# Optimization experiments

Hardware: AMD Instinct MI355X
Metric: run time of the kernel (lower is better)

Reference implementation:

```python
import jax, jax.numpy as jnp
import numpy as np

N, D, V = 2048, 64, 2048


def setup_inputs() -> dict:
    key = jax.random.key(0)
    k_ids, k_emb, k_tree, k_map = jax.random.split(key, 4)
    language_ids = jax.random.randint(k_ids, (N,), 0, V)
    language_embeddings = jax.random.normal(k_emb, (N, D), dtype=jnp.float32)
    # symmetric distance tables, mimicking the symmetric try/except dict lookup
    t = jax.random.uniform(k_tree, (V, V), dtype=jnp.float32)
    tree_dist = (t + t.T) * 0.5
    m = jax.random.uniform(k_map, (V, V), dtype=jnp.float32)
    map_dist = (m + m.T) * 0.5
    return {
        "language_ids": language_ids,
        "language_embeddings": language_embeddings,
        "tree_dist": tree_dist,
        "map_dist": map_dist,
    }


def reference(language_ids, language_embeddings, tree_dist, map_dist):
    # pairwise mean-L1 distance between embeddings: [N, N]
    emb_dist = jnp.mean(
        jnp.abs(language_embeddings[:, None, :] - language_embeddings[None, :, :]),
        axis=-1,
    )
    # largest_value_map_dist as computed in __init__
    largest = jnp.max(map_dist)
    ii = language_ids[:, None]  # [N, 1]
    jj = language_ids[None, :]  # [1, N]
    metric = (tree_dist[ii, jj] + map_dist[ii, jj] / largest) * 0.5  # [N, N]
    # pairs with equal language ids are skipped in the original loop
    mask = (ii != jj).astype(emb_dist.dtype)
    per_pair = jnp.abs(emb_dist - metric) * mask
    return jnp.sum(per_pair) / jnp.sum(mask)
```

## Files before the change

### kernel.cpp

```cpp
#include <hip/hip_runtime.h>
#include <hip/hip_bf16.h>

#define NL 2048
#define DE 64
#define VV 2048
#define BI 64
#define BJ 32
#define NTI (NL / BI)
#define NTJ (NL / BJ)
#define NBLK 1056
#define STI 68
#define STJ 36


__global__ __launch_bounds__(1024) void prep_kernel(const int* __restrict__ ids,
                                                    const float4* __restrict__ m4,
                                                    float* __restrict__ pmax,
                                                    int* __restrict__ perm,
                                                    int* __restrict__ sids) {
    const int t = threadIdx.x;
    const int lane = t & 63, wave = t >> 6;
    const int b = blockIdx.x;

    if (b < 256) {
        const float4* p = m4 + (size_t)b * 4096;
        const float4 x0 = p[t], x1 = p[t + 1024], x2 = p[t + 2048], x3 = p[t + 3072];
        float v = fmaxf(fmaxf(fmaxf(x0.x, x0.y), fmaxf(x0.z, x0.w)),
                        fmaxf(fmaxf(x1.x, x1.y), fmaxf(x1.z, x1.w)));
        v = fmaxf(v, fmaxf(fmaxf(x2.x, x2.y), fmaxf(x2.z, x2.w)));
        v = fmaxf(v, fmaxf(fmaxf(x3.x, x3.y), fmaxf(x3.z, x3.w)));
        #pragma unroll
        for (int o = 32; o > 0; o >>= 1)
            v = fmaxf(v, __shfl_down(v, o));
        __shared__ float wl[16];
        if (lane == 0) wl[wave] = v;
        __syncthreads();
        if (t == 0) {
            float m = wl[0];
            #pragma unroll
            for (int i = 1; i < 16; ++i) m = fmaxf(m, wl[i]);
            pmax[b] = m;
        }
    } else {
        __shared__ unsigned hist[VV];
        __shared__ unsigned offs[VV];
        __shared__ unsigned wtot[16];
        __shared__ unsigned wexc[16];
        hist[2 * t] = 0u; hist[2 * t + 1] = 0u;
        __syncthreads();
        const int id0 = ids[2 * t], id1 = ids[2 * t + 1];
        atomicAdd(&hist[id0], 1u);
        atomicAdd(&hist[id1], 1u);
        __syncthreads();
        const unsigned h0 = hist[2 * t], h1 = hist[2 * t + 1];
        const unsigned s = h0 + h1;
        unsigned ps = s;
        #pragma unroll
        for (int o = 1; o < 64; o <<= 1) {
            unsigned u = __shfl_up(ps, o);
            if (lane >= o) ps += u;
        }
        if (lane == 63) wtot[wave] = ps;
        __syncthreads();
        if (wave == 0 && lane < 16) {
            unsigned v = wtot[lane];
            unsigned pv = v;
            #pragma unroll
            for (int o = 1; o < 16; o <<= 1) {
                unsigned u = __shfl_up(pv, o);
                if (lane >= o) pv += u;
            }
            wexc[lane] = pv - v;
        }
        __syncthreads();
        const unsigned ex = wexc[wave] + ps - s;
        offs[2 * t]     = ex;
        offs[2 * t + 1] = ex + h0;
        __syncthreads();
        unsigned p0 = atomicAdd(&offs[id0], 1u);
        perm[p0] = 2 * t;     sids[p0] = id0;
        unsigned p1 = atomicAdd(&offs[id1], 1u);
        perm[p1] = 2 * t + 1; sids[p1] = id1;
    }
}

__global__ __launch_bounds__(256) void loss_kernel(
    const float* __restrict__ emb,
    const float* __restrict__ tree, const float* __restrict__ mapd,
    const int* __restrict__ perm, const int* __restrict__ sids,
    const float* __restrict__ pmax,
    float* __restrict__ psum, unsigned* __restrict__ pcnt)
{
    const int t = threadIdx.x;

    const int L = blockIdx.x;
    int bi = (int)((65.0f - sqrtf(4225.0f - 4.0f * (float)L)) * 0.5f);
    if (bi > NTI - 1) bi = NTI - 1;
    if (bi < 0) bi = 0;
    while (65 * bi - bi * bi > L) --bi;
    while (65 * (bi + 1) - (bi + 1) * (bi + 1) <= L) ++bi;
    const int bj = 2 * bi + (L - (65 * bi - bi * bi));

    __shared__ __align__(16) float Eit[DE][STI];
    __shared__ __align__(16) float Ejt[DE][STJ];
    __shared__ int idi[BI];
    __shared__ int idj[BJ];
    __shared__ float wm[4];

    float pv = pmax[t];

    {
        const int r  = t & 63;
        const int c0 = (t >> 6) << 4;
        const int gi = perm[bi * BI + r];
        const float4* pa = (const float4*)(emb + (size_t)gi * DE + c0);
        float4 a0 = pa[0], a1 = pa[1], a2 = pa[2], a3 = pa[3];
        Eit[c0 + 0][r]  = a0.x; Eit[c0 + 1][r]  = a0.y; Eit[c0 + 2][r]  = a0.z; Eit[c0 + 3][r]  = a0.w;
        Eit[c0 + 4][r]  = a1.x; Eit[c0 + 5][r]  = a1.y; Eit[c0 + 6][r]  = a1.z; Eit[c0 + 7][r]  = a1.w;
        Eit[c0 + 8][r]  = a2.x; Eit[c0 + 9][r]  = a2.y; Eit[c0 + 10][r] = a2.z; Eit[c0 + 11][r] = a2.w;
        Eit[c0 + 12][r] = a3.x; Eit[c0 + 13][r] = a3.y; Eit[c0 + 14][r] = a3.z; Eit[c0 + 15][r] = a3.w;

        const int rj  = t & 31;
        const int cj0 = (t >> 5) << 3;
        const int gj = perm[bj * BJ + rj];
        const float4* pb = (const float4*)(emb + (size_t)gj * DE + cj0);
        float4 b0 = pb[0], b1 = pb[1];
        Ejt[cj0 + 0][rj] = b0.x; Ejt[cj0 + 1][rj] = b0.y; Ejt[cj0 + 2][rj] = b0.z; Ejt[cj0 + 3][rj] = b0.w;
        Ejt[cj0 + 4][rj] = b1.x; Ejt[cj0 + 5][rj] = b1.y; Ejt[cj0 + 6][rj] = b1.z; Ejt[cj0 + 7][rj] = b1.w;

        if (t < BI)            idi[t] = sids[bi * BI + t];
        else if (t < BI + BJ)  idj[t - BI] = sids[bj * BJ + (t - BI)];
    }
    #pragma unroll
    for (int o = 32; o > 0; o >>= 1)
        pv = fmaxf(pv, __shfl_down(pv, o));
    if ((t & 63) == 0) wm[t >> 6] = pv;
    __syncthreads();

    const float inv = 1.0f / fmaxf(fmaxf(wm[0], wm[1]), fmaxf(wm[2], wm[3]));

    const int i0 = (t >> 4) * 4;
    const int j0 = (t & 15) * 2;

    int ia[4], ja[2];
    #pragma unroll
    for (int s = 0; s < 4; ++s) ia[s] = idi[i0 + s];
    #pragma unroll
    for (int c = 0; c < 2; ++c) ja[c] = idj[j0 + c];
    float tg[4][2], mg[4][2];
    #pragma unroll
    for (int s = 0; s < 4; ++s)
        #pragma unroll
        for (int c = 0; c < 2; ++c) {
            const int off = ia[s] * VV + ja[c];
            tg[s][c] = tree[off];
            mg[s][c] = mapd[off];
        }

    float acc[4][2];
    #pragma unroll
    for (int s = 0; s < 4; ++s) { acc[s][0] = 0.0f; acc[s][1] = 0.0f; }

    #pragma unroll 2
    for (int k = 0; k < 16; ++k) {
        #pragma unroll
        for (int q = 0; q < 4; ++q) {
            const int d = 4 * k + q;
            const float4 a = *(const float4*)&Eit[d][i0];
            const float2 b = *(const float2*)&Ejt[d][j0];
            acc[0][0] += fabsf(a.x - b.x); acc[0][1] += fabsf(a.x - b.y);
            acc[1][0] += fabsf(a.y - b.x); acc[1][1] += fabsf(a.y - b.y);
            acc[2][0] += fabsf(a.z - b.x); acc[2][1] += fabsf(a.z - b.y);
            acc[3][0] += fabsf(a.w - b.x); acc[3][1] += fabsf(a.w - b.y);
        }
    }

    float pp = 0.0f;
    unsigned cnt = 0;
    #pragma unroll
    for (int s = 0; s < 4; ++s) {
        const int posi = bi * BI + i0 + s;
        #pragma unroll
        for (int c = 0; c < 2; ++c) {
            const int posj = bj * BJ + j0 + c;
            if (posi < posj && ia[s] != ja[c]) {
                const float metric = (tg[s][c] + mg[s][c] * inv) * 0.5f;
                pp += 2.0f * fabsf(acc[s][c] * (1.0f / (float)DE) - metric);
                cnt += 2u;
            }
        }
    }

    #pragma unroll
    for (int o = 32; o > 0; o >>= 1) {
        pp  += __shfl_down(pp, o);
        cnt += __shfl_down(cnt, o);
    }
    __shared__ float    wsum_l[4];
    __shared__ unsigned wcnt_l[4];
    if ((t & 63) == 0) { wsum_l[t >> 6] = pp; wcnt_l[t >> 6] = cnt; }
    __syncthreads();
    if (t == 0) {
        psum[L] = wsum_l[0] + wsum_l[1] + wsum_l[2] + wsum_l[3];
        pcnt[L] = wcnt_l[0] + wcnt_l[1] + wcnt_l[2] + wcnt_l[3];
    }
}

__global__ __launch_bounds__(1024) void finalize_kernel(const float* __restrict__ psum,
                                                        const unsigned* __restrict__ pcnt,
                                                        float* __restrict__ out) {
    const int t = threadIdx.x;
    const int lane = t & 63, wave = t >> 6;
    double s = 0.0;
    unsigned c = 0;
    for (int i = t; i < NBLK; i += 1024) { s += (double)psum[i]; c += pcnt[i]; }
    #pragma unroll
    for (int o = 32; o > 0; o >>= 1) {
        s += __shfl_down(s, o);
        c += __shfl_down(c, o);
    }
    __shared__ double   sl[16];
    __shared__ unsigned cl[16];
    if (lane == 0) { sl[wave] = s; cl[wave] = c; }
    __syncthreads();
    if (t == 0) {
        double   S = sl[0];
        unsigned C = cl[0];
        #pragma unroll
        for (int i = 1; i < 16; ++i) { S += sl[i]; C += cl[i]; }
        out[0] = (float)(S / (double)C);
    }
}

extern "C" void kernel_launch(void* const* d_in, const int* in_sizes, int n_in,
                              void* d_out, int out_size, void* d_ws, size_t ws_size,
                              hipStream_t stream) {
    const int*   ids  = (const int*)d_in[0];
    const float* emb  = (const float*)d_in[1];
    const float* tree = (const float*)d_in[2];
    const float* mapd = (const float*)d_in[3];
    float* out = (float*)d_out;

    float*    pmax = (float*)d_ws;
    int*      perm = (int*)((char*)d_ws + 1024);
    int*      sids = (int*)((char*)d_ws + 9216);
    float*    psum = (float*)((char*)d_ws + 17408);
    unsigned* pcnt = (unsigned*)((char*)d_ws + 21632);

    prep_kernel<<<257, 1024, 0, stream>>>(ids, (const float4*)mapd, pmax, perm, sids);

    loss_kernel<<<NBLK, 256, 0, stream>>>(emb, tree, mapd, perm, sids, pmax, psum, pcnt);

    finalize_kernel<<<1, 1024, 0, stream>>>(psum, pcnt, out);
}
```

Measured before the change: 98.79 us.

## Enlarge i-tile to 128 with 4x4 register blocking and hoisted gathers

Doubles the i tile (BI 64→128) so each thread computes a 4x4 block of pairs instead of 4x2, halving the number of triangular blocks and increasing LDS reuse per load. The id and distance-table gathers are now issued straight from global memory before the embedding staging, rather than after the barrier, so their latency overlaps the shared-memory fill. Mask and metric are precomputed into a bitmask with popcount for the count. In exchange register pressure rises (a 3-waves hint is added), and fewer blocks means less parallelism across CUs.

```diff
diff --git a/kernel.cpp b/kernel.cpp
--- a/kernel.cpp
+++ b/kernel.cpp
@@ -4,12 +4,11 @@
 #define NL 2048
 #define DE 64
 #define VV 2048
-#define BI 64
+#define BI 128
 #define BJ 32
-#define NTI (NL / BI)
-#define NTJ (NL / BJ)
-#define NBLK 1056
-#define STI 68
+#define NTI 16
+#define NBLK 544
+#define STI 132
 #define STJ 36
 
 
@@ -84,7 +83,7 @@
     }
 }
 
-__global__ __launch_bounds__(256) void loss_kernel(
+__global__ __launch_bounds__(256, 3) void loss_kernel(
     const float* __restrict__ emb,
     const float* __restrict__ tree, const float* __restrict__ mapd,
     const int* __restrict__ perm, const int* __restrict__ sids,
@@ -94,24 +93,42 @@
     const int t = threadIdx.x;
 
     const int L = blockIdx.x;
-    int bi = (int)((65.0f - sqrtf(4225.0f - 4.0f * (float)L)) * 0.5f);
+    int bi = (int)((66.0f - sqrtf(4356.0f - 8.0f * (float)L)) * 0.25f);
     if (bi > NTI - 1) bi = NTI - 1;
     if (bi < 0) bi = 0;
-    while (65 * bi - bi * bi > L) --bi;
-    while (65 * (bi + 1) - (bi + 1) * (bi + 1) <= L) ++bi;
-    const int bj = 2 * bi + (L - (65 * bi - bi * bi));
+    while (66 * bi - 2 * bi * bi > L) --bi;
+    while (66 * (bi + 1) - 2 * (bi + 1) * (bi + 1) <= L) ++bi;
+    const int bj = 4 * bi + (L - (66 * bi - 2 * bi * bi));
+
+    const int i0 = (t >> 3) * 4;
+    const int j0 = (t & 7) * 4;
+
+    int ia[4], ja[4];
+    #pragma unroll
+    for (int s = 0; s < 4; ++s) ia[s] = sids[bi * BI + i0 + s];
+    #pragma unroll
+    for (int c = 0; c < 4; ++c) ja[c] = sids[bj * BJ + j0 + c];
+    float tg[4][4], mg[4][4];
+    #pragma unroll
+    for (int s = 0; s < 4; ++s)
+        #pragma unroll
+        for (int c = 0; c < 4; ++c) {
+            const int off = ia[s] * VV + ja[c];
+            tg[s][c] = tree[off];
+            mg[s][c] = mapd[off];
+        }
 
     __shared__ __align__(16) float Eit[DE][STI];
     __shared__ __align__(16) float Ejt[DE][STJ];
-    __shared__ int idi[BI];
-    __shared__ int idj[BJ];
     __shared__ float wm[4];
 
     float pv = pmax[t];
 
-    {
-        const int r  = t & 63;
-        const int c0 = (t >> 6) << 4;
+    #pragma unroll
+    for (int s = 0; s < 2; ++s) {
+        const int idx = t + 256 * s;
+        const int r  = idx & 127;
+        const int c0 = (idx >> 7) * 16;
         const int gi = perm[bi * BI + r];
         const float4* pa = (const float4*)(emb + (size_t)gi * DE + c0);
         float4 a0 = pa[0], a1 = pa[1], a2 = pa[2], a3 = pa[3];
@@ -119,17 +136,17 @@
         Eit[c0 + 4][r]  = a1.x; Eit[c0 + 5][r]  = a1.y; Eit[c0 + 6][r]  = a1.z; Eit[c0 + 7][r]  = a1.w;
         Eit[c0 + 8][r]  = a2.x; Eit[c0 + 9][r]  = a2.y; Eit[c0 + 10][r] = a2.z; Eit[c0 + 11][r] = a2.w;
         Eit[c0 + 12][r] = a3.x; Eit[c0 + 13][r] = a3.y; Eit[c0 + 14][r] = a3.z; Eit[c0 + 15][r] = a3.w;
-
-        const int rj  = t & 31;
-        const int cj0 = (t >> 5) << 3;
-        const int gj = perm[bj * BJ + rj];
-        const float4* pb = (const float4*)(emb + (size_t)gj * DE + cj0);
-        float4 b0 = pb[0], b1 = pb[1];
-        Ejt[cj0 + 0][rj] = b0.x; Ejt[cj0 + 1][rj] = b0.y; Ejt[cj0 + 2][rj] = b0.z; Ejt[cj0 + 3][rj] = b0.w;
-        Ejt[cj0 + 4][rj] = b1.x; Ejt[cj0 + 5][rj] = b1.y; Ejt[cj0 + 6][rj] = b1.z; Ejt[cj0 + 7][rj] = b1.w;
-
-        if (t < BI)            idi[t] = sids[bi * BI + t];
-        else if (t < BI + BJ)  idj[t - BI] = sids[bj * BJ + (t - BI)];
+    }
+    if (t < 128) {
+        const int r  = t & 31;
+        const int c0 = (t >> 5) * 16;
+        const int gj = perm[bj * BJ + r];
+        const float4* pb = (const float4*)(emb + (size_t)gj * DE + c0);
+        float4 b0 = pb[0], b1 = pb[1], b2 = pb[2], b3 = pb[3];
+        Ejt[c0 + 0][r]  = b0.x; Ejt[c0 + 1][r]  = b0.y; Ejt[c0 + 2][r]  = b0.z; Ejt[c0 + 3][r]  = b0.w;
+        Ejt[c0 + 4][r]  = b1.x; Ejt[c0 + 5][r]  = b1.y; Ejt[c0 + 6][r]  = b1.z; Ejt[c0 + 7][r]  = b1.w;
+        Ejt[c0 + 8][r]  = b2.x; Ejt[c0 + 9][r]  = b2.y; Ejt[c0 + 10][r] = b2.z; Ejt[c0 + 11][r] = b2.w;
+        Ejt[c0 + 12][r] = b3.x; Ejt[c0 + 13][r] = b3.y; Ejt[c0 + 14][r] = b3.z; Ejt[c0 + 15][r] = b3.w;
     }
     #pragma unroll
     for (int o = 32; o > 0; o >>= 1)
@@ -139,27 +156,24 @@
 
     const float inv = 1.0f / fmaxf(fmaxf(wm[0], wm[1]), fmaxf(wm[2], wm[3]));
 
-    const int i0 = (t >> 4) * 4;
-    const int j0 = (t & 15) * 2;
-
-    int ia[4], ja[2];
-    #pragma unroll
-    for (int s = 0; s < 4; ++s) ia[s] = idi[i0 + s];
-    #pragma unroll
-    for (int c = 0; c < 2; ++c) ja[c] = idj[j0 + c];
-    float tg[4][2], mg[4][2];
+    float met[4][4];
+    unsigned mbits = 0u;
+    #pragma unroll
+    for (int s = 0; s < 4; ++s) {
+        const int posi = bi * BI + i0 + s;
+        #pragma unroll
+        for (int c = 0; c < 4; ++c) {
+            met[s][c] = 0.5f * (tg[s][c] + mg[s][c] * inv);
+            const int posj = bj * BJ + j0 + c;
+            if (posi < posj && ia[s] != ja[c]) mbits |= 1u << (s * 4 + c);
+        }
+    }
+
+    float acc[4][4];
     #pragma unroll
     for (int s = 0; s < 4; ++s)
         #pragma unroll
-        for (int c = 0; c < 2; ++c) {
-            const int off = ia[s] * VV + ja[c];
-            tg[s][c] = tree[off];
-            mg[s][c] = mapd[off];
-        }
-
-    float acc[4][2];
-    #pragma unroll
-    for (int s = 0; s < 4; ++s) { acc[s][0] = 0.0f; acc[s][1] = 0.0f; }
+        for (int c = 0; c < 4; ++c) acc[s][c] = 0.0f;
 
     #pragma unroll 2
     for (int k = 0; k < 16; ++k) {
@@ -167,29 +181,26 @@
         for (int q = 0; q < 4; ++q) {
             const int d = 4 * k + q;
             const float4 a = *(const float4*)&Eit[d][i0];
-            const float2 b = *(const float2*)&Ejt[d][j0];
+            const float4 b = *(const float4*)&Ejt[d][j0];
             acc[0][0] += fabsf(a.x - b.x); acc[0][1] += fabsf(a.x - b.y);
+            acc[0][2] += fabsf(a.x - b.z); acc[0][3] += fabsf(a.x - b.w);
             acc[1][0] += fabsf(a.y - b.x); acc[1][1] += fabsf(a.y - b.y);
+            acc[1][2] += fabsf(a.y - b.z); acc[1][3] += fabsf(a.y - b.w);
             acc[2][0] += fabsf(a.z - b.x); acc[2][1] += fabsf(a.z - b.y);
+            acc[2][2] += fabsf(a.z - b.z); acc[2][3] += fabsf(a.z - b.w);
             acc[3][0] += fabsf(a.w - b.x); acc[3][1] += fabsf(a.w - b.y);
+            acc[3][2] += fabsf(a.w - b.z); acc[3][3] += fabsf(a.w - b.w);
         }
     }
 
     float pp = 0.0f;
-    unsigned cnt = 0;
-    #pragma unroll
-    for (int s = 0; s < 4; ++s) {
-        const int posi = bi * BI + i0 + s;
-        #pragma unroll
-        for (int c = 0; c < 2; ++c) {
-            const int posj = bj * BJ + j0 + c;
-            if (posi < posj && ia[s] != ja[c]) {
-                const float metric = (tg[s][c] + mg[s][c] * inv) * 0.5f;
-                pp += 2.0f * fabsf(acc[s][c] * (1.0f / (float)DE) - metric);
-                cnt += 2u;
-            }
-        }
-    }
+    #pragma unroll
+    for (int s = 0; s < 4; ++s)
+        #pragma unroll
+        for (int c = 0; c < 4; ++c)
+            if (mbits & (1u << (s * 4 + c)))
+                pp += 2.0f * fabsf(acc[s][c] * (1.0f / (float)DE) - met[s][c]);
+    unsigned cnt = 2u * (unsigned)__popc(mbits);
 
     #pragma unroll
     for (int o = 32; o > 0; o >>= 1) {
```

New measurement: 105.3 us. 1.07x slower.
